# Kernel tuning notes

Measured on AMD Instinct MI355X. Metric: run time of the kernel, lower is better.

The kernel has to match this reference:

```python
import jax, jax.numpy as jnp
import numpy as np

B, N, D, H = 256, 1000, 128, 8
DH = D // H
TANH_CLIP = 10.0
NEG = -1e9  # finite stand-in for -inf mask fill (keeps grads clean)


def setup_inputs() -> dict:
    key = jax.random.key(0)
    ks = jax.random.split(key, 8)
    s = 1.0 / np.sqrt(D)
    return {
        "node_embeddings": jax.random.normal(ks[0], (B, N, D), jnp.float32),
        "W_node": jax.random.normal(ks[1], (D, 3 * D), jnp.float32) * s,   # project_node_embeddings
        "W_fixed": jax.random.normal(ks[2], (D, D), jnp.float32) * s,      # project_fixed_context
        "W_step": jax.random.normal(ks[3], (2 * D, D), jnp.float32) * s,   # project_step_context
        "W_out": jax.random.normal(ks[4], (D, D), jnp.float32) * s,        # project_out
        "prev_idx": jax.random.randint(ks[5], (B,), 0, N),
        "first_idx": jax.random.randint(ks[6], (B,), 0, N),
        "mask": jax.random.randint(ks[7], (B, N), 0, 2).astype(bool),      # True = masked/visited
    }


def reference(node_embeddings, W_node, W_fixed, W_step, W_out, prev_idx, first_idx, mask):
    b = jnp.arange(B)
    # Precompute fixed: context projection of graph embedding (mean aggregation)
    graph_embed = node_embeddings.mean(axis=1)                    # (B, D)
    fixed_context = graph_embed @ W_fixed                          # (B, D)
    # glimpse key / glimpse val / logit key from node embeddings
    kvl = node_embeddings @ W_node                                 # (B, N, 3D)
    glimpse_K, glimpse_V, logit_K = jnp.split(kvl, 3, axis=-1)
    gK = glimpse_K.reshape(B, N, H, DH)                            # (B, N, H, dh)
    gV = glimpse_V.reshape(B, N, H, DH)
    # Step context: cat(first node embed, last node embed) -> query
    step_ctx = jnp.concatenate(
        [node_embeddings[b, first_idx], node_embeddings[b, prev_idx]], axis=-1)  # (B, 2D)
    query = fixed_context + step_ctx @ W_step                      # (B, D)
    Q = query.reshape(B, H, DH)                                    # (B, H, dh)
    # Glimpse MHA (single query per batch element)
    compat = jnp.einsum("bhd,bnhd->bhn", Q, gK) / np.sqrt(DH)      # (B, H, N)
    compat = jnp.where(mask[:, None, :], NEG, compat)              # mask_inner
    attn = jax.nn.softmax(compat, axis=-1)
    heads = jnp.einsum("bhn,bnhd->bhd", attn, gV)                  # (B, H, dh)
    glimpse = heads.reshape(B, D) @ W_out                          # (B, D)
    # Logits against logit_K, tanh clipping, mask_logits, log-softmax
    logits = jnp.einsum("bd,bnd->bn", glimpse, logit_K) / np.sqrt(D)
    logits = TANH_CLIP * jnp.tanh(logits)
    logits = jnp.where(mask, NEG, logits)
    log_p = jax.nn.log_softmax(logits, axis=-1)                    # (B, N)
    return log_p
```

## Files before the change

kernel.cpp:

```cpp
#include <hip/hip_runtime.h>
#include <math.h>

#define BB 256
#define NN 1000
#define DD 128
#define HH 8
#define CC 8
#define RC 125
#define NEG -1e9f

__device__ __forceinline__ bool get_mask(const void* m, int flag, size_t idx) {
    if (flag == 1) return ((const int*)m)[idx] != 0;
    if (flag == 2) return ((const float*)m)[idx] != 0.0f;
    return ((const unsigned char*)m)[idx] != 0;
}

__global__ __launch_bounds__(256) void k_mean(
        const float* __restrict__ X, float* __restrict__ partial,
        const unsigned int* __restrict__ maskw, int* __restrict__ flag) {
    int bid = blockIdx.x, tid = threadIdx.x;
    int b = bid >> 3, ch = bid & 7;
    if (bid == 0 && tid < 64) {
        unsigned int a0 = maskw[tid], a1 = maskw[tid + 64],
                     a2 = maskw[tid + 128], a3 = maskw[tid + 192];
        int ii = (a0 <= 1u) && (a1 <= 1u) && (a2 <= 1u) && (a3 <= 1u);
        int ff = (a0 == 0u || a0 == 0x3F800000u) && (a1 == 0u || a1 == 0x3F800000u) &&
                 (a2 == 0u || a2 == 0x3F800000u) && (a3 == 0u || a3 == 0x3F800000u);
        int ai = __all(ii), af = __all(ff);
        if (tid == 0) *flag = ai ? 1 : (af ? 2 : 0);
    }
    int c = tid & 31, s = tid >> 5;
    const float4* Xr = (const float4*)(X + (size_t)b * NN * DD);
    float4 acc = make_float4(0.f, 0.f, 0.f, 0.f);
    int n0 = ch * RC;
    for (int nl = s; nl < RC; nl += 8) {
        float4 v = Xr[(n0 + nl) * 32 + c];
        acc.x += v.x; acc.y += v.y; acc.z += v.z; acc.w += v.w;
    }
    __shared__ float4 red[8][32];
    red[s][c] = acc;
    __syncthreads();
    for (int st = 4; st >= 1; st >>= 1) {
        if (s < st) {
            float4 o = red[s + st][c];
            red[s][c].x += o.x; red[s][c].y += o.y;
            red[s][c].z += o.z; red[s][c].w += o.w;
        }
        __syncthreads();
    }
    if (s == 0) {
        float4 r = red[0][c];
        float* outp = partial + ((size_t)b * CC + ch) * DD + 4 * c;
        outp[0] = r.x; outp[1] = r.y; outp[2] = r.z; outp[3] = r.w;
    }
}

__global__ __launch_bounds__(256) void k_qk(
        const float* __restrict__ X, const float* __restrict__ Wfix,
        const float* __restrict__ Wstep, const float* __restrict__ Wnode,
        const float* __restrict__ partial, const int* __restrict__ prev,
        const int* __restrict__ first, float* __restrict__ qkg) {
    int b = blockIdx.x, tid = threadIdx.x;
    const size_t xoff = (size_t)b * NN * DD;
    __shared__ float ge[DD], sc[2 * DD], qv[DD], qp[2][DD];
    if (tid < DD) {
        float g = 0.f;
        #pragma unroll
        for (int ch = 0; ch < CC; ++ch) g += partial[((size_t)b * CC + ch) * DD + tid];
        ge[tid] = g * (1.0f / NN);
    }
    {
        int src = (tid < DD) ? first[b] : prev[b];
        sc[tid] = X[xoff + (size_t)src * DD + (tid & 127)];
    }
    __syncthreads();
    int p = tid >> 7, d = tid & 127;
    {
        float a = 0.f;
        #pragma unroll 4
        for (int k = p * 64; k < p * 64 + 64; ++k)      a += ge[k] * Wfix[(size_t)k * DD + d];
        #pragma unroll 4
        for (int k = p * 128; k < p * 128 + 128; ++k)   a += sc[k] * Wstep[(size_t)k * DD + d];
        qp[p][d] = a;
    }
    __syncthreads();
    if (tid < DD) qv[tid] = qp[0][tid] + qp[1][tid];
    __syncthreads();
    {
        const float* wrow = Wnode + (size_t)d * 384;
        #pragma unroll
        for (int h = p * 4; h < p * 4 + 4; ++h) {
            const float4* wr = (const float4*)(wrow + h * 16);
            float a = 0.f;
            #pragma unroll
            for (int j4 = 0; j4 < 4; ++j4) {
                float4 w = wr[j4];
                a += w.x * qv[h * 16 + 4 * j4]     + w.y * qv[h * 16 + 4 * j4 + 1]
                   + w.z * qv[h * 16 + 4 * j4 + 2] + w.w * qv[h * 16 + 4 * j4 + 3];
            }
            qkg[((size_t)b * HH + h) * DD + d] = 0.25f * a;
        }
    }
}

__global__ __launch_bounds__(256, 8) void k_flash(
        const float* __restrict__ X, const float* __restrict__ qkg,
        const void* __restrict__ mask, const int* __restrict__ flag,
        float* __restrict__ mqw, float* __restrict__ sqw,
        float* __restrict__ pvp) {
    int bid = blockIdx.x, tid = threadIdx.x;
    int b = bid >> 3, ch = bid & 7;
    const int n0 = ch * RC;
    const size_t xoff = (size_t)b * NN * DD;
    const int f = *flag;

    __shared__ float qk[HH][DD];
    __shared__ float cm[HH][RC + 3];
    __shared__ float mloc[HH];
    __shared__ float xp[2][HH][DD];

    for (int i = tid; i < HH * DD; i += 256)
        qk[i >> 7][i & 127] = qkg[(size_t)b * HH * DD + i];
    __syncthreads();

    {
        int g = tid & 7, r = tid >> 3;
        #pragma unroll
        for (int it = 0; it < 4; ++it) {
            int nl = it * 32 + r;
            if (it < 3 || nl < RC) {
                int n = n0 + nl;
                const float4* xr = (const float4*)(X + xoff + (size_t)n * DD);
                float acc[HH] = {0.f, 0.f, 0.f, 0.f, 0.f, 0.f, 0.f, 0.f};
                #pragma unroll
                for (int i = 0; i < 4; ++i) {
                    float4 v = xr[g + 8 * i];
                    int col = 4 * (g + 8 * i);
                    #pragma unroll
                    for (int h = 0; h < HH; ++h)
                        acc[h] += v.x * qk[h][col]     + v.y * qk[h][col + 1]
                                + v.z * qk[h][col + 2] + v.w * qk[h][col + 3];
                }
                #pragma unroll
                for (int h = 0; h < HH; ++h) {
                    acc[h] += __shfl_xor(acc[h], 1, 8);
                    acc[h] += __shfl_xor(acc[h], 2, 8);
                    acc[h] += __shfl_xor(acc[h], 4, 8);
                }
                float val = acc[0];
                #pragma unroll
                for (int h = 1; h < HH; ++h) val = (g == h) ? acc[h] : val;
                bool mk = get_mask(mask, f, (size_t)b * NN + n);
                cm[g][nl] = mk ? NEG : val;
            }
        }
    }
    __syncthreads();

    {
        int h = tid >> 5, l = tid & 31;
        float mx = -INFINITY;
        for (int nl = l; nl < RC; nl += 32) mx = fmaxf(mx, cm[h][nl]);
        #pragma unroll
        for (int off = 16; off >= 1; off >>= 1) mx = fmaxf(mx, __shfl_xor(mx, off, 32));
        if (l == 0) mloc[h] = mx;
    }
    __syncthreads();

    {
        int h = tid >> 5, l = tid & 31;
        float m_h = mloc[h];
        float sm = 0.f;
        for (int nl = l; nl < RC; nl += 32) {
            float p = __expf(cm[h][nl] - m_h);
            cm[h][nl] = p;
            sm += p;
        }
        #pragma unroll
        for (int off = 16; off >= 1; off >>= 1) sm += __shfl_xor(sm, off, 32);
        if (l == 0) {
            sqw[((size_t)b * CC + ch) * HH + h] = sm;
            mqw[((size_t)b * CC + ch) * HH + h] = m_h;
        }
    }
    __syncthreads();

    {
        int s2 = tid >> 7, d = tid & 127;
        float acc[HH] = {0.f, 0.f, 0.f, 0.f, 0.f, 0.f, 0.f, 0.f};
        #pragma unroll 2
        for (int nl = s2; nl < RC; nl += 2) {
            float x = X[xoff + (size_t)(n0 + nl) * DD + d];
            #pragma unroll
            for (int h = 0; h < HH; ++h) acc[h] += cm[h][nl] * x;
        }
        #pragma unroll
        for (int h = 0; h < HH; ++h) xp[s2][h][d] = acc[h];
        __syncthreads();
        if (s2 == 0) {
            #pragma unroll
            for (int h = 0; h < HH; ++h)
                pvp[(((size_t)b * CC + ch) * HH + h) * DD + d] = xp[0][h][d] + xp[1][h][d];
        }
    }
}

__global__ __launch_bounds__(256) void k_comb(
        const float* __restrict__ Wnode, const float* __restrict__ Wout,
        const float* __restrict__ mqw, const float* __restrict__ sqw,
        const float* __restrict__ pvp, float* __restrict__ gqg) {
    int b = blockIdx.x, tid = threadIdx.x;
    __shared__ float wq[CC][HH], Sh[HH];
    __shared__ float xa[HH][DD], qp[2][DD], hd[DD], gl[DD];
    if (tid < HH) {
        float m = mqw[((size_t)b * CC) * HH + tid];
        #pragma unroll
        for (int ch = 1; ch < CC; ++ch)
            m = fmaxf(m, mqw[((size_t)b * CC + ch) * HH + tid]);
        float S = 0.f;
        #pragma unroll
        for (int ch = 0; ch < CC; ++ch) {
            float wgt = __expf(mqw[((size_t)b * CC + ch) * HH + tid] - m);
            wq[ch][tid] = wgt;
            S += sqw[((size_t)b * CC + ch) * HH + tid] * wgt;
        }
        Sh[tid] = 1.0f / S;
    }
    __syncthreads();
    for (int idx = tid; idx < HH * DD; idx += 256) {
        int h = idx >> 7, d = idx & 127;
        float a = 0.f;
        #pragma unroll
        for (int ch = 0; ch < CC; ++ch)
            a += pvp[(((size_t)b * CC + ch) * HH + h) * DD + d] * wq[ch][h];
        xa[h][d] = a * Sh[h];
    }
    __syncthreads();
    int p = tid >> 7, t = tid & 127;
    {
        int h = t >> 4;
        float a = 0.f;
        #pragma unroll 4
        for (int d = p * 64; d < p * 64 + 64; ++d)
            a += xa[h][d] * Wnode[(size_t)d * 384 + 128 + t];
        qp[p][t] = a;
    }
    __syncthreads();
    if (tid < DD) hd[tid] = qp[0][tid] + qp[1][tid];
    __syncthreads();
    {
        float a = 0.f;
        #pragma unroll 4
        for (int k = p * 64; k < p * 64 + 64; ++k) a += hd[k] * Wout[(size_t)k * DD + t];
        qp[p][t] = a;
    }
    __syncthreads();
    if (tid < DD) gl[tid] = qp[0][tid] + qp[1][tid];
    __syncthreads();
    {
        const float4* wr = (const float4*)(Wnode + (size_t)t * 384 + 256 + p * 64);
        float a = 0.f;
        #pragma unroll
        for (int j4 = 0; j4 < 16; ++j4) {
            float4 w = wr[j4];
            int k = p * 64 + 4 * j4;
            a += w.x * gl[k] + w.y * gl[k + 1] + w.z * gl[k + 2] + w.w * gl[k + 3];
        }
        qp[p][t] = a;
    }
    __syncthreads();
    if (tid < DD) gqg[(size_t)b * DD + tid] = (qp[0][tid] + qp[1][tid]) * 0.08838834764831845f;
}

__global__ __launch_bounds__(256, 8) void k_logits(
        const float* __restrict__ X, const float* __restrict__ gqg,
        const void* __restrict__ mask, const int* __restrict__ flag,
        float* __restrict__ lg, float* __restrict__ esumg) {
    int bid = blockIdx.x, tid = threadIdx.x;
    int b = bid >> 3, ch = bid & 7;
    const int n0 = ch * RC;
    const size_t xoff = (size_t)b * NN * DD;
    const int f = *flag;
    __shared__ float gqv[DD];
    __shared__ float redw[4];
    if (tid < DD) gqv[tid] = gqg[(size_t)b * DD + tid];
    __syncthreads();
    int g = tid & 7, r = tid >> 3;
    float esum = 0.f;
    #pragma unroll
    for (int it = 0; it < 4; ++it) {
        int nl = it * 32 + r;
        if (it < 3 || nl < RC) {
            int n = n0 + nl;
            const float4* xr = (const float4*)(X + xoff + (size_t)n * DD);
            float a = 0.f;
            #pragma unroll
            for (int i = 0; i < 4; ++i) {
                float4 v = xr[g + 8 * i];
                int col = 4 * (g + 8 * i);
                a += v.x * gqv[col] + v.y * gqv[col + 1]
                   + v.z * gqv[col + 2] + v.w * gqv[col + 3];
            }
            a += __shfl_xor(a, 1, 8);
            a += __shfl_xor(a, 2, 8);
            a += __shfl_xor(a, 4, 8);
            if (g == 0) {
                float l = 10.0f * tanhf(a);
                if (get_mask(mask, f, (size_t)b * NN + n)) l = NEG;
                lg[(size_t)b * NN + n] = l;
                esum += __expf(l - 10.0f);
            }
        }
    }
    #pragma unroll
    for (int off = 32; off >= 1; off >>= 1) esum += __shfl_xor(esum, off, 64);
    if ((tid & 63) == 0) redw[tid >> 6] = esum;
    __syncthreads();
    if (tid == 0) esumg[(size_t)b * CC + ch] = redw[0] + redw[1] + redw[2] + redw[3];
}

__global__ __launch_bounds__(256) void k_final(
        const float* __restrict__ lg, const float* __restrict__ esumg,
        float* __restrict__ out) {
    int b = blockIdx.x, tid = threadIdx.x;
    float s = 0.f;
    #pragma unroll
    for (int ch = 0; ch < CC; ++ch) s += esumg[(size_t)b * CC + ch];
    float lse = 10.0f + logf(s);
    for (int n = tid; n < NN; n += 256)
        out[(size_t)b * NN + n] = lg[(size_t)b * NN + n] - lse;
}

__global__ __launch_bounds__(1024) void k_mega(
        const float* __restrict__ X, const float* __restrict__ Wnode,
        const float* __restrict__ Wfix, const float* __restrict__ Wstep,
        const float* __restrict__ Wout, const int* __restrict__ prev,
        const int* __restrict__ first, const void* __restrict__ mask,
        float* __restrict__ out) {
    int b = blockIdx.x, tid = threadIdx.x;
    __shared__ __align__(16) float cm[HH * 1024];
    __shared__ __align__(16) float qkl[HH * DD];
    __shared__ __align__(16) float qpart[8 * DD];
    __shared__ float xa[HH * DD];
    __shared__ float ge[DD], q[DD], sc[2 * DD], hd[DD], gl[DD], gqv[DD];
    __shared__ float red[16], invh[8];
    __shared__ int s_flag;
    const size_t xoff = (size_t)b * NN * DD;

    if (tid < 64) {
        const unsigned int* mw = (const unsigned int*)mask;
        unsigned int a0 = mw[tid], a1 = mw[tid + 64], a2 = mw[tid + 128], a3 = mw[tid + 192];
        int ii = (a0 <= 1u) && (a1 <= 1u) && (a2 <= 1u) && (a3 <= 1u);
        int ff = (a0 == 0u || a0 == 0x3F800000u) && (a1 == 0u || a1 == 0x3F800000u) &&
                 (a2 == 0u || a2 == 0x3F800000u) && (a3 == 0u || a3 == 0x3F800000u);
        int ai = __all(ii), af = __all(ff);
        if (tid == 0) s_flag = ai ? 1 : (af ? 2 : 0);
    }
    if (tid >= 256 && tid < 512) {
        int t = tid - 256;
        int src = (t < DD) ? first[b] : prev[b];
        sc[t] = X[xoff + (size_t)src * DD + (t & 127)];
    }
    {
        float4* red4 = (float4*)cm;
        int c = tid & 31, s = tid >> 5;
        const float4* Xr = (const float4*)(X + xoff);
        float4 acc = make_float4(0.f, 0.f, 0.f, 0.f);
        for (int n = s; n < NN; n += 32) {
            float4 v = Xr[n * 32 + c];
            acc.x += v.x; acc.y += v.y; acc.z += v.z; acc.w += v.w;
        }
        red4[s * 32 + c] = acc;
        __syncthreads();
        for (int st = 16; st >= 1; st >>= 1) {
            if (s < st) {
                float4 o = red4[(s + st) * 32 + c];
                float4 r = red4[s * 32 + c];
                r.x += o.x; r.y += o.y; r.z += o.z; r.w += o.w;
                red4[s * 32 + c] = r;
            }
            __syncthreads();
        }
        if (s == 0) {
            float4 r = red4[c];
            ge[4 * c] = r.x * (1.0f / NN); ge[4 * c + 1] = r.y * (1.0f / NN);
            ge[4 * c + 2] = r.z * (1.0f / NN); ge[4 * c + 3] = r.w * (1.0f / NN);
        }
        __syncthreads();
    }
    const int flag = s_flag;
    {
        int p = tid >> 7, d = tid & 127;
        float a = 0.f;
        for (int k = p * 16; k < p * 16 + 16; ++k) a += ge[k] * Wfix[k * DD + d];
        for (int k = p * 32; k < p * 32 + 32; ++k) a += sc[k] * Wstep[k * DD + d];
        qpart[p * DD + d] = a;
        __syncthreads();
        if (tid < DD) {
            float s = 0.f;
            for (int pp = 0; pp < 8; ++pp) s += qpart[pp * DD + tid];
            q[tid] = s;
        }
        __syncthreads();
        int d2 = tid >> 3, h = tid & 7;
        const float4* wr = (const float4*)(Wnode + (size_t)d2 * 384 + h * 16);
        float a2 = 0.f;
        for (int j4 = 0; j4 < 4; ++j4) {
            float4 w = wr[j4];
            a2 += w.x * q[h * 16 + 4 * j4]     + w.y * q[h * 16 + 4 * j4 + 1]
                + w.z * q[h * 16 + 4 * j4 + 2] + w.w * q[h * 16 + 4 * j4 + 3];
        }
        qkl[h * DD + d2] = 0.25f * a2;
        __syncthreads();
    }
    {
        int g = tid & 7;
        for (int it = 0; it < 8; ++it) {
            int n = it * 128 + (tid >> 3);
            if (n < NN) {
                float acc[HH] = {0.f, 0.f, 0.f, 0.f, 0.f, 0.f, 0.f, 0.f};
                const float4* xr = (const float4*)(X + xoff + (size_t)n * DD);
                for (int i = 0; i < 4; ++i) {
                    float4 v = xr[g + 8 * i];
                    int col = 4 * (g + 8 * i);
                    for (int h = 0; h < HH; ++h)
                        acc[h] += v.x * qkl[h * DD + col]     + v.y * qkl[h * DD + col + 1]
                                + v.z * qkl[h * DD + col + 2] + v.w * qkl[h * DD + col + 3];
                }
                for (int h = 0; h < HH; ++h) {
                    acc[h] += __shfl_xor(acc[h], 1, 8);
                    acc[h] += __shfl_xor(acc[h], 2, 8);
                    acc[h] += __shfl_xor(acc[h], 4, 8);
                }
                float val = acc[0];
                for (int h = 1; h < HH; ++h) val = (g == h) ? acc[h] : val;
                bool mk = get_mask(mask, flag, (size_t)b * NN + n);
                cm[g * 1024 + n] = mk ? NEG : val;
            }
        }
        __syncthreads();
    }
    {
        int h = tid >> 7, lane = tid & 127;
        float mx = -INFINITY;
        for (int n = lane; n < NN; n += 128) mx = fmaxf(mx, cm[h * 1024 + n]);
        for (int off = 32; off >= 1; off >>= 1) mx = fmaxf(mx, __shfl_xor(mx, off, 64));
        if ((tid & 63) == 0) red[tid >> 6] = mx;
        __syncthreads();
        float m_h = fmaxf(red[2 * h], red[2 * h + 1]);
        float sm = 0.f;
        for (int n = lane; n < NN; n += 128) {
            float p = __expf(cm[h * 1024 + n] - m_h);
            cm[h * 1024 + n] = p;
            sm += p;
        }
        for (int off = 32; off >= 1; off >>= 1) sm += __shfl_xor(sm, off, 64);
        __syncthreads();
        if ((tid & 63) == 0) red[tid >> 6] = sm;
        __syncthreads();
        if (tid < HH) invh[tid] = 1.0f / (red[2 * tid] + red[2 * tid + 1]);
        __syncthreads();
    }
    {
        int s = tid >> 7, d = tid & 127;
        float acc[HH] = {0.f, 0.f, 0.f, 0.f, 0.f, 0.f, 0.f, 0.f};
        for (int n = s; n < NN; n += 8) {
            float x = X[xoff + (size_t)n * DD + d];
            for (int h = 0; h < HH; ++h) acc[h] += cm[h * 1024 + n] * x;
        }
        __syncthreads();
        float* xp = cm;
        for (int h = 0; h < HH; ++h) xp[(s * HH + h) * DD + d] = acc[h];
        __syncthreads();
        if (s == 0) {
            for (int h = 0; h < HH; ++h) {
                float t = 0.f;
                for (int ss = 0; ss < 8; ++ss) t += xp[(ss * HH + h) * DD + d];
                xa[h * DD + d] = t * invh[h];
            }
        }
        __syncthreads();
    }
    {
        int p = tid >> 7, t = tid & 127;
        int h = t >> 4;
        float a = 0.f;
        for (int d = p * 16; d < p * 16 + 16; ++d)
            a += xa[h * DD + d] * Wnode[(size_t)d * 384 + 128 + t];
        qpart[p * DD + t] = a;
        __syncthreads();
        if (tid < DD) {
            float s = 0.f;
            for (int pp = 0; pp < 8; ++pp) s += qpart[pp * DD + tid];
            hd[tid] = s;
        }
        __syncthreads();
        a = 0.f;
        for (int k = p * 16; k < p * 16 + 16; ++k) a += hd[k] * Wout[(size_t)k * DD + t];
        qpart[p * DD + t] = a;
        __syncthreads();
        if (tid < DD) {
            float s = 0.f;
            for (int pp = 0; pp < 8; ++pp) s += qpart[pp * DD + tid];
            gl[tid] = s;
        }
        __syncthreads();
        const float4* wr = (const float4*)(Wnode + (size_t)t * 384 + 256 + p * 16);
        a = 0.f;
        for (int j4 = 0; j4 < 4; ++j4) {
            float4 w = wr[j4];
            int k = p * 16 + 4 * j4;
            a += w.x * gl[k] + w.y * gl[k + 1] + w.z * gl[k + 2] + w.w * gl[k + 3];
        }
        qpart[p * DD + t] = a;
        __syncthreads();
        if (tid < DD) {
            float s = 0.f;
            for (int pp = 0; pp < 8; ++pp) s += qpart[pp * DD + tid];
            gqv[tid] = s * 0.08838834764831845f;
        }
        __syncthreads();
    }
    {
        float* lg = qkl;
        int g = tid & 7;
        for (int it = 0; it < 8; ++it) {
            int n = it * 128 + (tid >> 3);
            if (n < NN) {
                const float4* xr = (const float4*)(X + xoff + (size_t)n * DD);
                float a = 0.f;
                for (int i = 0; i < 4; ++i) {
                    float4 v = xr[g + 8 * i];
                    int col = 4 * (g + 8 * i);
                    a += v.x * gqv[col] + v.y * gqv[col + 1] + v.z * gqv[col + 2] + v.w * gqv[col + 3];
                }
                a += __shfl_xor(a, 1, 8);
                a += __shfl_xor(a, 2, 8);
                a += __shfl_xor(a, 4, 8);
                if (g == 0) {
                    float lgt = 10.0f * tanhf(a);
                    lg[n] = get_mask(mask, flag, (size_t)b * NN + n) ? NEG : lgt;
                }
            }
        }
        __syncthreads();
        float v = (tid < NN) ? lg[tid] : -INFINITY;
        float mx = v;
        for (int off = 32; off >= 1; off >>= 1) mx = fmaxf(mx, __shfl_xor(mx, off, 64));
        if ((tid & 63) == 0) red[tid >> 6] = mx;
        __syncthreads();
        float m = red[0];
        for (int w = 1; w < 16; ++w) m = fmaxf(m, red[w]);
        float e = (tid < NN) ? __expf(v - m) : 0.f;
        float sm = e;
        for (int off = 32; off >= 1; off >>= 1) sm += __shfl_xor(sm, off, 64);
        __syncthreads();
        if ((tid & 63) == 0) red[tid >> 6] = sm;
        __syncthreads();
        float s2 = 0.f;
        for (int w = 0; w < 16; ++w) s2 += red[w];
        float lse = m + logf(s2);
        if (tid < NN) out[(size_t)b * NN + tid] = v - lse;
    }
}

extern "C" void kernel_launch(void* const* d_in, const int* in_sizes, int n_in,
                              void* d_out, int out_size, void* d_ws, size_t ws_size,
                              hipStream_t stream) {
    const float* X     = (const float*)d_in[0];
    const float* Wnode = (const float*)d_in[1];
    const float* Wfix  = (const float*)d_in[2];
    const float* Wstep = (const float*)d_in[3];
    const float* Wout  = (const float*)d_in[4];
    const int*   prev  = (const int*)d_in[5];
    const int*   first = (const int*)d_in[6];
    const void*  mask  = d_in[7];
    float* out = (float*)d_out;

    char* wsb = (char*)d_ws;
    int*   flag    = (int*)wsb;
    float* base    = (float*)(wsb + 256);
    float* partial = base;
    float* qkg     = partial + (size_t)BB * CC * DD;
    float* mqw     = qkg + (size_t)BB * HH * DD;
    float* sqw     = mqw + (size_t)BB * CC * HH;
    float* pvp     = sqw + (size_t)BB * CC * HH;
    float* gqg     = pvp + (size_t)BB * CC * HH * DD;
    float* esumg   = gqg + (size_t)BB * DD;
    float* lg      = esumg + (size_t)BB * CC;
    const size_t need = 256 + sizeof(float) * (
        (size_t)BB * CC * DD + (size_t)BB * HH * DD + 2 * (size_t)BB * CC * HH +
        (size_t)BB * CC * HH * DD + (size_t)BB * DD + (size_t)BB * CC + (size_t)BB * NN);

    if (ws_size >= need) {
        k_mean  <<<BB * CC, 256, 0, stream>>>(X, partial, (const unsigned int*)mask, flag);
        k_qk    <<<BB, 256, 0, stream>>>(X, Wfix, Wstep, Wnode, partial, prev, first, qkg);
        k_flash <<<BB * CC, 256, 0, stream>>>(X, qkg, mask, flag, mqw, sqw, pvp);
        k_comb  <<<BB, 256, 0, stream>>>(Wnode, Wout, mqw, sqw, pvp, gqg);
        k_logits<<<BB * CC, 256, 0, stream>>>(X, gqg, mask, flag, lg, esumg);
        k_final <<<BB, 256, 0, stream>>>(lg, esumg, out);
    } else {
        k_mega<<<BB, 1024, 0, stream>>>(X, Wnode, Wfix, Wstep, Wout,
                                        prev, first, mask, out);
    }
}
```

Baseline: 125.9 us.

## Stage node embeddings as bf16 copy during mean pass for later kernels

The mean-reduction kernel now also writes a bf16 copy of the node embeddings into workspace, and the flash-attention and logits kernels read that half-size copy instead of the fp32 input. This targets the memory traffic of re-reading the full 131 MB embedding tensor in two later passes. The cost is an extra 65 MB write, a larger workspace requirement, and reduced precision in the attention and logit dot products. If the workspace is too small, the code falls back to the mega kernel.

```diff
diff --git a/kernel.cpp b/kernel.cpp
--- a/kernel.cpp
+++ b/kernel.cpp
@@ -8,15 +8,25 @@
 #define CC 8
 #define RC 125
 #define NEG -1e9f
-
+#define CMS 132
+
+__device__ __forceinline__ float bf2f(unsigned int u) {
+    return __uint_as_float(u << 16);
+}
+__device__ __forceinline__ unsigned short f2bf(float f) {
+    unsigned int u = __float_as_uint(f);
+    u += 0x7FFFu + ((u >> 16) & 1u);
+    return (unsigned short)(u >> 16);
+}
 __device__ __forceinline__ bool get_mask(const void* m, int flag, size_t idx) {
     if (flag == 1) return ((const int*)m)[idx] != 0;
     if (flag == 2) return ((const float*)m)[idx] != 0.0f;
     return ((const unsigned char*)m)[idx] != 0;
 }
 
-__global__ __launch_bounds__(256) void k_mean(
+__global__ __launch_bounds__(256, 8) void k_stage(
         const float* __restrict__ X, float* __restrict__ partial,
+        unsigned short* __restrict__ Xb,
         const unsigned int* __restrict__ maskw, int* __restrict__ flag) {
     int bid = blockIdx.x, tid = threadIdx.x;
     int b = bid >> 3, ch = bid & 7;
@@ -31,11 +41,17 @@
     }
     int c = tid & 31, s = tid >> 5;
     const float4* Xr = (const float4*)(X + (size_t)b * NN * DD);
+    uint2* Xw = (uint2*)Xb;
     float4 acc = make_float4(0.f, 0.f, 0.f, 0.f);
     int n0 = ch * RC;
     for (int nl = s; nl < RC; nl += 8) {
-        float4 v = Xr[(n0 + nl) * 32 + c];
+        int n = n0 + nl;
+        float4 v = Xr[n * 32 + c];
         acc.x += v.x; acc.y += v.y; acc.z += v.z; acc.w += v.w;
+        uint2 p;
+        p.x = (unsigned)f2bf(v.x) | ((unsigned)f2bf(v.y) << 16);
+        p.y = (unsigned)f2bf(v.z) | ((unsigned)f2bf(v.w) << 16);
+        Xw[((size_t)b * NN + n) * 32 + c] = p;
     }
     __shared__ float4 red[8][32];
     red[s][c] = acc;
@@ -104,18 +120,17 @@
 }
 
 __global__ __launch_bounds__(256, 8) void k_flash(
-        const float* __restrict__ X, const float* __restrict__ qkg,
+        const unsigned short* __restrict__ Xb, const float* __restrict__ qkg,
         const void* __restrict__ mask, const int* __restrict__ flag,
         float* __restrict__ mqw, float* __restrict__ sqw,
         float* __restrict__ pvp) {
     int bid = blockIdx.x, tid = threadIdx.x;
     int b = bid >> 3, ch = bid & 7;
     const int n0 = ch * RC;
-    const size_t xoff = (size_t)b * NN * DD;
     const int f = *flag;
 
     __shared__ float qk[HH][DD];
-    __shared__ float cm[HH][RC + 3];
+    __shared__ float cm[HH][CMS];
     __shared__ float mloc[HH];
     __shared__ float xp[2][HH][DD];
 
@@ -130,16 +145,17 @@
             int nl = it * 32 + r;
             if (it < 3 || nl < RC) {
                 int n = n0 + nl;
-                const float4* xr = (const float4*)(X + xoff + (size_t)n * DD);
+                const uint4* xr = (const uint4*)(Xb + ((size_t)b * NN + n) * DD);
+                uint4 c0 = xr[g], c1 = xr[g + 8];
+                unsigned int wsv[8] = {c0.x, c0.y, c0.z, c0.w, c1.x, c1.y, c1.z, c1.w};
                 float acc[HH] = {0.f, 0.f, 0.f, 0.f, 0.f, 0.f, 0.f, 0.f};
                 #pragma unroll
-                for (int i = 0; i < 4; ++i) {
-                    float4 v = xr[g + 8 * i];
-                    int col = 4 * (g + 8 * i);
+                for (int i = 0; i < 8; ++i) {
+                    int col = (i < 4) ? (8 * g + 2 * i) : (64 + 8 * g + 2 * (i - 4));
+                    float lo = bf2f(wsv[i] & 0xffffu), hi = bf2f(wsv[i] >> 16);
                     #pragma unroll
                     for (int h = 0; h < HH; ++h)
-                        acc[h] += v.x * qk[h][col]     + v.y * qk[h][col + 1]
-                                + v.z * qk[h][col + 2] + v.w * qk[h][col + 3];
+                        acc[h] += lo * qk[h][col] + hi * qk[h][col + 1];
                 }
                 #pragma unroll
                 for (int h = 0; h < HH; ++h) {
@@ -188,9 +204,8 @@
     {
         int s2 = tid >> 7, d = tid & 127;
         float acc[HH] = {0.f, 0.f, 0.f, 0.f, 0.f, 0.f, 0.f, 0.f};
-        #pragma unroll 2
         for (int nl = s2; nl < RC; nl += 2) {
-            float x = X[xoff + (size_t)(n0 + nl) * DD + d];
+            float x = bf2f((unsigned int)Xb[((size_t)b * NN + n0 + nl) * DD + d]);
             #pragma unroll
             for (int h = 0; h < HH; ++h) acc[h] += cm[h][nl] * x;
         }
@@ -273,13 +288,12 @@
 }
 
 __global__ __launch_bounds__(256, 8) void k_logits(
-        const float* __restrict__ X, const float* __restrict__ gqg,
+        const unsigned short* __restrict__ Xb, const float* __restrict__ gqg,
         const void* __restrict__ mask, const int* __restrict__ flag,
         float* __restrict__ lg, float* __restrict__ esumg) {
     int bid = blockIdx.x, tid = threadIdx.x;
     int b = bid >> 3, ch = bid & 7;
     const int n0 = ch * RC;
-    const size_t xoff = (size_t)b * NN * DD;
     const int f = *flag;
     __shared__ float gqv[DD];
     __shared__ float redw[4];
@@ -292,14 +306,14 @@
         int nl = it * 32 + r;
         if (it < 3 || nl < RC) {
             int n = n0 + nl;
-            const float4* xr = (const float4*)(X + xoff + (size_t)n * DD);
+            const uint4* xr = (const uint4*)(Xb + ((size_t)b * NN + n) * DD);
+            uint4 c0 = xr[g], c1 = xr[g + 8];
+            unsigned int wsv[8] = {c0.x, c0.y, c0.z, c0.w, c1.x, c1.y, c1.z, c1.w};
             float a = 0.f;
             #pragma unroll
-            for (int i = 0; i < 4; ++i) {
-                float4 v = xr[g + 8 * i];
-                int col = 4 * (g + 8 * i);
-                a += v.x * gqv[col] + v.y * gqv[col + 1]
-                   + v.z * gqv[col + 2] + v.w * gqv[col + 3];
+            for (int i = 0; i < 8; ++i) {
+                int col = (i < 4) ? (8 * g + 2 * i) : (64 + 8 * g + 2 * (i - 4));
+                a += bf2f(wsv[i] & 0xffffu) * gqv[col] + bf2f(wsv[i] >> 16) * gqv[col + 1];
             }
             a += __shfl_xor(a, 1, 8);
             a += __shfl_xor(a, 2, 8);
@@ -579,8 +593,7 @@
 
     char* wsb = (char*)d_ws;
     int*   flag    = (int*)wsb;
-    float* base    = (float*)(wsb + 256);
-    float* partial = base;
+    float* partial = (float*)(wsb + 256);
     float* qkg     = partial + (size_t)BB * CC * DD;
     float* mqw     = qkg + (size_t)BB * HH * DD;
     float* sqw     = mqw + (size_t)BB * CC * HH;
@@ -588,16 +601,19 @@
     float* gqg     = pvp + (size_t)BB * CC * HH * DD;
     float* esumg   = gqg + (size_t)BB * DD;
     float* lg      = esumg + (size_t)BB * CC;
-    const size_t need = 256 + sizeof(float) * (
+    const size_t fl_end = 256 + sizeof(float) * (
         (size_t)BB * CC * DD + (size_t)BB * HH * DD + 2 * (size_t)BB * CC * HH +
         (size_t)BB * CC * HH * DD + (size_t)BB * DD + (size_t)BB * CC + (size_t)BB * NN);
+    const size_t xb_off = (fl_end + 255) & ~(size_t)255;
+    unsigned short* Xb = (unsigned short*)(wsb + xb_off);
+    const size_t need = xb_off + (size_t)2 * BB * NN * DD;
 
     if (ws_size >= need) {
-        k_mean  <<<BB * CC, 256, 0, stream>>>(X, partial, (const unsigned int*)mask, flag);
+        k_stage <<<BB * CC, 256, 0, stream>>>(X, partial, Xb, (const unsigned int*)mask, flag);
         k_qk    <<<BB, 256, 0, stream>>>(X, Wfix, Wstep, Wnode, partial, prev, first, qkg);
-        k_flash <<<BB * CC, 256, 0, stream>>>(X, qkg, mask, flag, mqw, sqw, pvp);
+        k_flash <<<BB * CC, 256, 0, stream>>>(Xb, qkg, mask, flag, mqw, sqw, pvp);
         k_comb  <<<BB, 256, 0, stream>>>(Wnode, Wout, mqw, sqw, pvp, gqg);
-        k_logits<<<BB * CC, 256, 0, stream>>>(X, gqg, mask, flag, lg, esumg);
+        k_logits<<<BB * CC, 256, 0, stream>>>(Xb, gqg, mask, flag, lg, esumg);
         k_final <<<BB, 256, 0, stream>>>(lg, esumg, out);
     } else {
         k_mega<<<BB, 1024, 0, stream>>>(X, Wnode, Wfix, Wstep, Wout,
```

After: 131.4 us. 1.04x slower.

## Compact unmasked node indices and skip masked rows in attention and logits

Applied to the files above, without the earlier changes.

k_qk now stream-compacts the unmasked node indices per batch with a ballot and prefix count, storing a count and an index list. k_flash and k_logits iterate only over unmasked rows, spreading them evenly across the eight chunks, so the X reads and dot products for masked nodes (about half) are skipped. k_flash also becomes single-pass: it drops the running max and clamps scores to 80 before exp, which removes the mqw rescaling in k_comb. In exchange it relies on scores staying bounded to avoid overflow, adds a gather through the index list, and fully masked rows would divide by a zero sum.

```diff
diff --git a/kernel.cpp b/kernel.cpp
--- a/kernel.cpp
+++ b/kernel.cpp
@@ -59,10 +59,16 @@
         const float* __restrict__ X, const float* __restrict__ Wfix,
         const float* __restrict__ Wstep, const float* __restrict__ Wnode,
         const float* __restrict__ partial, const int* __restrict__ prev,
-        const int* __restrict__ first, float* __restrict__ qkg) {
+        const int* __restrict__ first, const void* __restrict__ mask,
+        const int* __restrict__ flag, float* __restrict__ qkg,
+        unsigned short* __restrict__ cidx, int* __restrict__ cnt) {
     int b = blockIdx.x, tid = threadIdx.x;
     const size_t xoff = (size_t)b * NN * DD;
+    const int f = *flag;
     __shared__ float ge[DD], sc[2 * DD], qv[DD], qp[2][DD];
+    __shared__ int wbase[4];
+    __shared__ int s_total;
+
     if (tid < DD) {
         float g = 0.f;
         #pragma unroll
@@ -73,6 +79,7 @@
         int src = (tid < DD) ? first[b] : prev[b];
         sc[tid] = X[xoff + (size_t)src * DD + (tid & 127)];
     }
+    if (tid == 0) s_total = 0;
     __syncthreads();
     int p = tid >> 7, d = tid & 127;
     {
@@ -101,129 +108,134 @@
             qkg[((size_t)b * HH + h) * DD + d] = 0.25f * a;
         }
     }
-}
-
-__global__ __launch_bounds__(256, 8) void k_flash(
+    int w = tid >> 6, lane = tid & 63;
+    for (int seg = 0; seg < 4; ++seg) {
+        int n = seg * 256 + tid;
+        bool un = (n < NN) && !get_mask(mask, f, (size_t)b * NN + n);
+        unsigned long long bal = __ballot(un);
+        if (lane == 0) wbase[w] = __popcll(bal);
+        __syncthreads();
+        int base = s_total;
+        for (int ww = 0; ww < w; ++ww) base += wbase[ww];
+        int myoff = __popcll(bal & ((1ULL << lane) - 1ULL));
+        if (un) cidx[(size_t)b * 1024 + base + myoff] = (unsigned short)n;
+        __syncthreads();
+        if (tid == 0) s_total += wbase[0] + wbase[1] + wbase[2] + wbase[3];
+        __syncthreads();
+    }
+    if (tid == 0) cnt[b] = s_total;
+}
+
+__global__ __launch_bounds__(256, 4) void k_flash(
         const float* __restrict__ X, const float* __restrict__ qkg,
-        const void* __restrict__ mask, const int* __restrict__ flag,
-        float* __restrict__ mqw, float* __restrict__ sqw,
-        float* __restrict__ pvp) {
+        const unsigned short* __restrict__ cidx, const int* __restrict__ cnt,
+        float* __restrict__ sqw, float* __restrict__ pvp) {
     int bid = blockIdx.x, tid = threadIdx.x;
     int b = bid >> 3, ch = bid & 7;
-    const int n0 = ch * RC;
     const size_t xoff = (size_t)b * NN * DD;
-    const int f = *flag;
-
-    __shared__ float qk[HH][DD];
-    __shared__ float cm[HH][RC + 3];
-    __shared__ float mloc[HH];
-    __shared__ float xp[2][HH][DD];
+
+    __shared__ __align__(16) float qks[HH][DD];
+    __shared__ __align__(16) float redpv[4][HH][DD];
+    __shared__ float redS[4][HH];
 
     for (int i = tid; i < HH * DD; i += 256)
-        qk[i >> 7][i & 127] = qkg[(size_t)b * HH * DD + i];
-    __syncthreads();
-
-    {
-        int g = tid & 7, r = tid >> 3;
-        #pragma unroll
-        for (int it = 0; it < 4; ++it) {
-            int nl = it * 32 + r;
-            if (it < 3 || nl < RC) {
-                int n = n0 + nl;
-                const float4* xr = (const float4*)(X + xoff + (size_t)n * DD);
-                float acc[HH] = {0.f, 0.f, 0.f, 0.f, 0.f, 0.f, 0.f, 0.f};
+        qks[i >> 7][i & 127] = qkg[(size_t)b * HH * DD + i];
+    __syncthreads();
+
+    const int g = tid & 15;
+    const int r = tid >> 4;
+    const int w = tid >> 6;
+
+    int total = cnt[b];
+    int rpc = (total + CC - 1) / CC;
+    int k0 = ch * rpc;
+    int k1 = k0 + rpc; if (k1 > total) k1 = total;
+    int len = k1 - k0; if (len < 0) len = 0;
+    int iters = (len + 15) >> 4;
+
+    float acc[HH][8];
+    #pragma unroll
+    for (int h = 0; h < HH; ++h)
+        #pragma unroll
+        for (int j = 0; j < 8; ++j) acc[h][j] = 0.f;
+    float S[HH] = {0.f, 0.f, 0.f, 0.f, 0.f, 0.f, 0.f, 0.f};
+
+    for (int it = 0; it < iters; ++it) {
+        int k = k0 + it * 16 + r;
+        if (k < k1) {
+            int n = cidx[(size_t)b * 1024 + k];
+            const float4* xr = (const float4*)(X + xoff + (size_t)n * DD + 8 * g);
+            float4 v0 = xr[0], v1 = xr[1];
+            float v[8] = {v0.x, v0.y, v0.z, v0.w, v1.x, v1.y, v1.z, v1.w};
+            float cp[HH];
+            #pragma unroll
+            for (int h = 0; h < HH; ++h) {
+                const float4* qr = (const float4*)&qks[h][8 * g];
+                float4 q0 = qr[0], q1 = qr[1];
+                cp[h] = v[0] * q0.x + v[1] * q0.y + v[2] * q0.z + v[3] * q0.w
+                      + v[4] * q1.x + v[5] * q1.y + v[6] * q1.z + v[7] * q1.w;
+            }
+            #pragma unroll
+            for (int h = 0; h < HH; ++h) {
+                cp[h] += __shfl_xor(cp[h], 1, 16);
+                cp[h] += __shfl_xor(cp[h], 2, 16);
+                cp[h] += __shfl_xor(cp[h], 4, 16);
+                cp[h] += __shfl_xor(cp[h], 8, 16);
+            }
+            #pragma unroll
+            for (int h = 0; h < HH; ++h) {
+                float pe = __expf(fminf(cp[h], 80.f));
+                S[h] += pe;
                 #pragma unroll
-                for (int i = 0; i < 4; ++i) {
-                    float4 v = xr[g + 8 * i];
-                    int col = 4 * (g + 8 * i);
-                    #pragma unroll
-                    for (int h = 0; h < HH; ++h)
-                        acc[h] += v.x * qk[h][col]     + v.y * qk[h][col + 1]
-                                + v.z * qk[h][col + 2] + v.w * qk[h][col + 3];
-                }
-                #pragma unroll
-                for (int h = 0; h < HH; ++h) {
-                    acc[h] += __shfl_xor(acc[h], 1, 8);
-                    acc[h] += __shfl_xor(acc[h], 2, 8);
-                    acc[h] += __shfl_xor(acc[h], 4, 8);
-                }
-                float val = acc[0];
-                #pragma unroll
-                for (int h = 1; h < HH; ++h) val = (g == h) ? acc[h] : val;
-                bool mk = get_mask(mask, f, (size_t)b * NN + n);
-                cm[g][nl] = mk ? NEG : val;
-            }
-        }
-    }
-    __syncthreads();
-
-    {
-        int h = tid >> 5, l = tid & 31;
-        float mx = -INFINITY;
-        for (int nl = l; nl < RC; nl += 32) mx = fmaxf(mx, cm[h][nl]);
-        #pragma unroll
-        for (int off = 16; off >= 1; off >>= 1) mx = fmaxf(mx, __shfl_xor(mx, off, 32));
-        if (l == 0) mloc[h] = mx;
-    }
-    __syncthreads();
-
-    {
-        int h = tid >> 5, l = tid & 31;
-        float m_h = mloc[h];
-        float sm = 0.f;
-        for (int nl = l; nl < RC; nl += 32) {
-            float p = __expf(cm[h][nl] - m_h);
-            cm[h][nl] = p;
-            sm += p;
-        }
-        #pragma unroll
-        for (int off = 16; off >= 1; off >>= 1) sm += __shfl_xor(sm, off, 32);
-        if (l == 0) {
-            sqw[((size_t)b * CC + ch) * HH + h] = sm;
-            mqw[((size_t)b * CC + ch) * HH + h] = m_h;
-        }
-    }
-    __syncthreads();
-
-    {
-        int s2 = tid >> 7, d = tid & 127;
-        float acc[HH] = {0.f, 0.f, 0.f, 0.f, 0.f, 0.f, 0.f, 0.f};
-        #pragma unroll 2
-        for (int nl = s2; nl < RC; nl += 2) {
-            float x = X[xoff + (size_t)(n0 + nl) * DD + d];
+                for (int j = 0; j < 8; ++j) acc[h][j] += pe * v[j];
+            }
+        }
+    }
+    #pragma unroll
+    for (int h = 0; h < HH; ++h) {
+        S[h] += __shfl_xor(S[h], 16, 64);
+        S[h] += __shfl_xor(S[h], 32, 64);
+        #pragma unroll
+        for (int j = 0; j < 8; ++j) {
+            acc[h][j] += __shfl_xor(acc[h][j], 16, 64);
+            acc[h][j] += __shfl_xor(acc[h][j], 32, 64);
+        }
+    }
+    if ((tid & 63) < 16) {
+        #pragma unroll
+        for (int h = 0; h < HH; ++h) {
+            *((float4*)&redpv[w][h][8 * g])     =
+                make_float4(acc[h][0], acc[h][1], acc[h][2], acc[h][3]);
+            *((float4*)&redpv[w][h][8 * g + 4]) =
+                make_float4(acc[h][4], acc[h][5], acc[h][6], acc[h][7]);
+        }
+        if (g == 0) {
             #pragma unroll
-            for (int h = 0; h < HH; ++h) acc[h] += cm[h][nl] * x;
-        }
-        #pragma unroll
-        for (int h = 0; h < HH; ++h) xp[s2][h][d] = acc[h];
-        __syncthreads();
-        if (s2 == 0) {
-            #pragma unroll
-            for (int h = 0; h < HH; ++h)
-                pvp[(((size_t)b * CC + ch) * HH + h) * DD + d] = xp[0][h][d] + xp[1][h][d];
-        }
-    }
+            for (int h = 0; h < HH; ++h) redS[w][h] = S[h];
+        }
+    }
+    __syncthreads();
+    for (int idx = tid; idx < HH * DD; idx += 256) {
+        int h = idx >> 7, d = idx & 127;
+        pvp[(((size_t)b * CC + ch) * HH + h) * DD + d] =
+            redpv[0][h][d] + redpv[1][h][d] + redpv[2][h][d] + redpv[3][h][d];
+    }
+    if (tid < HH)
+        sqw[((size_t)b * CC + ch) * HH + tid] =
+            redS[0][tid] + redS[1][tid] + redS[2][tid] + redS[3][tid];
 }
 
 __global__ __launch_bounds__(256) void k_comb(
         const float* __restrict__ Wnode, const float* __restrict__ Wout,
-        const float* __restrict__ mqw, const float* __restrict__ sqw,
-        const float* __restrict__ pvp, float* __restrict__ gqg) {
+        const float* __restrict__ sqw, const float* __restrict__ pvp,
+        float* __restrict__ gqg) {
     int b = blockIdx.x, tid = threadIdx.x;
-    __shared__ float wq[CC][HH], Sh[HH];
+    __shared__ float Sh[HH];
     __shared__ float xa[HH][DD], qp[2][DD], hd[DD], gl[DD];
     if (tid < HH) {
-        float m = mqw[((size_t)b * CC) * HH + tid];
-        #pragma unroll
-        for (int ch = 1; ch < CC; ++ch)
-            m = fmaxf(m, mqw[((size_t)b * CC + ch) * HH + tid]);
         float S = 0.f;
         #pragma unroll
-        for (int ch = 0; ch < CC; ++ch) {
-            float wgt = __expf(mqw[((size_t)b * CC + ch) * HH + tid] - m);
-            wq[ch][tid] = wgt;
-            S += sqw[((size_t)b * CC + ch) * HH + tid] * wgt;
-        }
+        for (int ch = 0; ch < CC; ++ch) S += sqw[((size_t)b * CC + ch) * HH + tid];
         Sh[tid] = 1.0f / S;
     }
     __syncthreads();
@@ -232,7 +244,7 @@
         float a = 0.f;
         #pragma unroll
         for (int ch = 0; ch < CC; ++ch)
-            a += pvp[(((size_t)b * CC + ch) * HH + h) * DD + d] * wq[ch][h];
+            a += pvp[(((size_t)b * CC + ch) * HH + h) * DD + d];
         xa[h][d] = a * Sh[h];
     }
     __syncthreads();
@@ -275,23 +287,31 @@
 __global__ __launch_bounds__(256, 8) void k_logits(
         const float* __restrict__ X, const float* __restrict__ gqg,
         const void* __restrict__ mask, const int* __restrict__ flag,
+        const unsigned short* __restrict__ cidx, const int* __restrict__ cnt,
         float* __restrict__ lg, float* __restrict__ esumg) {
     int bid = blockIdx.x, tid = threadIdx.x;
     int b = bid >> 3, ch = bid & 7;
-    const int n0 = ch * RC;
     const size_t xoff = (size_t)b * NN * DD;
     const int f = *flag;
     __shared__ float gqv[DD];
     __shared__ float redw[4];
     if (tid < DD) gqv[tid] = gqg[(size_t)b * DD + tid];
     __syncthreads();
-    int g = tid & 7, r = tid >> 3;
+    if (tid < RC) {
+        int n = ch * RC + tid;
+        if (get_mask(mask, f, (size_t)b * NN + n)) lg[(size_t)b * NN + n] = NEG;
+    }
+    int total = cnt[b];
+    int rpc = (total + CC - 1) / CC;
+    int k0 = ch * rpc, k1 = k0 + rpc; if (k1 > total) k1 = total;
+    int len = k1 - k0; if (len < 0) len = 0;
+    int iters = (len + 31) >> 5;
+    int g = tid & 7, rr = tid >> 3;
     float esum = 0.f;
-    #pragma unroll
-    for (int it = 0; it < 4; ++it) {
-        int nl = it * 32 + r;
-        if (it < 3 || nl < RC) {
-            int n = n0 + nl;
+    for (int it = 0; it < iters; ++it) {
+        int k = k0 + it * 32 + rr;
+        if (k < k1) {
+            int n = cidx[(size_t)b * 1024 + k];
             const float4* xr = (const float4*)(X + xoff + (size_t)n * DD);
             float a = 0.f;
             #pragma unroll
@@ -306,7 +326,6 @@
             a += __shfl_xor(a, 4, 8);
             if (g == 0) {
                 float l = 10.0f * tanhf(a);
-                if (get_mask(mask, f, (size_t)b * NN + n)) l = NEG;
                 lg[(size_t)b * NN + n] = l;
                 esum += __expf(l - 10.0f);
             }
@@ -579,25 +598,27 @@
 
     char* wsb = (char*)d_ws;
     int*   flag    = (int*)wsb;
-    float* base    = (float*)(wsb + 256);
-    float* partial = base;
+    float* partial = (float*)(wsb + 256);
     float* qkg     = partial + (size_t)BB * CC * DD;
-    float* mqw     = qkg + (size_t)BB * HH * DD;
-    float* sqw     = mqw + (size_t)BB * CC * HH;
+    float* sqw     = qkg + (size_t)BB * HH * DD;
     float* pvp     = sqw + (size_t)BB * CC * HH;
     float* gqg     = pvp + (size_t)BB * CC * HH * DD;
     float* esumg   = gqg + (size_t)BB * DD;
     float* lg      = esumg + (size_t)BB * CC;
+    int*   cnt     = (int*)(lg + (size_t)BB * NN);
+    unsigned short* cidx = (unsigned short*)(cnt + BB);
     const size_t need = 256 + sizeof(float) * (
-        (size_t)BB * CC * DD + (size_t)BB * HH * DD + 2 * (size_t)BB * CC * HH +
-        (size_t)BB * CC * HH * DD + (size_t)BB * DD + (size_t)BB * CC + (size_t)BB * NN);
+        (size_t)BB * CC * DD + (size_t)BB * HH * DD + (size_t)BB * CC * HH +
+        (size_t)BB * CC * HH * DD + (size_t)BB * DD + (size_t)BB * CC + (size_t)BB * NN)
+        + sizeof(int) * BB + sizeof(unsigned short) * (size_t)BB * 1024;
 
     if (ws_size >= need) {
         k_mean  <<<BB * CC, 256, 0, stream>>>(X, partial, (const unsigned int*)mask, flag);
-        k_qk    <<<BB, 256, 0, stream>>>(X, Wfix, Wstep, Wnode, partial, prev, first, qkg);
-        k_flash <<<BB * CC, 256, 0, stream>>>(X, qkg, mask, flag, mqw, sqw, pvp);
-        k_comb  <<<BB, 256, 0, stream>>>(Wnode, Wout, mqw, sqw, pvp, gqg);
-        k_logits<<<BB * CC, 256, 0, stream>>>(X, gqg, mask, flag, lg, esumg);
+        k_qk    <<<BB, 256, 0, stream>>>(X, Wfix, Wstep, Wnode, partial, prev, first,
+                                         mask, flag, qkg, cidx, cnt);
+        k_flash <<<BB * CC, 256, 0, stream>>>(X, qkg, cidx, cnt, sqw, pvp);
+        k_comb  <<<BB, 256, 0, stream>>>(Wnode, Wout, sqw, pvp, gqg);
+        k_logits<<<BB * CC, 256, 0, stream>>>(X, gqg, mask, flag, cidx, cnt, lg, esumg);
         k_final <<<BB, 256, 0, stream>>>(lg, esumg, out);
     } else {
         k_mega<<<BB, 1024, 0, stream>>>(X, Wnode, Wfix, Wstep, Wout,
```

After: 122.0 us. -3.1%, faster.
